# Performance work log

Hardware: AMD Instinct MI355X
Metric: run time of the kernel (lower is better)

## Reference

```python
import jax, jax.numpy as jnp
import numpy as np

B, D, K, A = 32768, 256, 1024, 32
MIN_LOG_STD, MAX_LOG_STD = -20.0, 2.0


def setup_inputs() -> dict:
    key = jax.random.key(0)
    ks = jax.random.split(key, 9)
    return {
        "obs": jax.random.normal(ks[0], (B, D), dtype=jnp.float32),
        "mean_C": jax.random.normal(ks[1], (K, D), dtype=jnp.float32),
        "mean_sigma": jnp.abs(jax.random.normal(ks[2], (K,), dtype=jnp.float32)) + 0.1,
        "mean_w": jax.random.normal(ks[3], (A, K), dtype=jnp.float32),
        "mean_b": jax.random.normal(ks[4], (A,), dtype=jnp.float32),
        "std_C": jax.random.normal(ks[5], (K, D), dtype=jnp.float32),
        "std_sigma": jnp.abs(jax.random.normal(ks[6], (K,), dtype=jnp.float32)) + 0.1,
        "std_w": jax.random.normal(ks[7], (A, K), dtype=jnp.float32),
        "std_b": jax.random.normal(ks[8], (A,), dtype=jnp.float32),
    }


def _rbf(x, C, sigma_sq, w, b):
    # r[b,k] = sum_d (x[b,d] - C[k,d])^2, expanded to avoid a [B,K,D] intermediate
    x2 = jnp.sum(x * x, axis=-1, keepdims=True)           # [B,1]
    c2 = jnp.sum(C * C, axis=-1)[None, :]                  # [1,K]
    r = x2 - 2.0 * (x @ C.T) + c2                          # [B,K]
    phi = jnp.exp(-r / (2.0 * jnp.abs(sigma_sq)[None, :]))  # [B,K]
    return phi @ w.T + b[None, :]                          # [B,A]


def reference(obs, mean_C, mean_sigma, mean_w, mean_b,
              std_C, std_sigma, std_w, std_b):
    action_mean = _rbf(obs, mean_C, mean_sigma, mean_w, mean_b)
    std_raw = _rbf(obs, std_C, std_sigma, std_w, std_b)
    action_std = jnp.exp(jnp.clip(std_raw, MIN_LOG_STD, MAX_LOG_STD))
    return jnp.concatenate((action_mean, action_std), axis=-1)  # [B, 2A]
```

## Files before the change

### kernel.cpp

```cpp
#include <hip/hip_runtime.h>


typedef float floatx4 __attribute__((ext_vector_type(4)));
typedef int   intx4  __attribute__((ext_vector_type(4)));
typedef unsigned int u32;
typedef unsigned char u8;

constexpr float LOG2E = 1.4426950408889634f;
constexpr float QS    = 25.4f;
constexpr float SINV2 = (5.0f / 127.0f) * (5.0f / 127.0f);

__device__ __forceinline__ u32 pk_fp8(float a, float b, float c, float d) {
  u32 v = __builtin_amdgcn_cvt_pk_fp8_f32(a, b, 0u, 0);
  v = __builtin_amdgcn_cvt_pk_fp8_f32(c, d, v, 1);
  return v;
}
__device__ __forceinline__ long mk64(u32 lo, u32 hi) {
  return (long)lo | ((long)hi << 32);
}
__device__ __forceinline__ int q8(float x) {
  return (int)rintf(fminf(fmaxf(x * QS, -127.f), 127.f));
}
__device__ __forceinline__ u32 pk_i8(int a, int b, int c, int d) {
  return (u32)(a & 255) | ((u32)(b & 255) << 8) | ((u32)(c & 255) << 16) | ((u32)(d & 255) << 24);
}

__global__ void prep(const float* __restrict__ mC, const float* __restrict__ mS,
                     const float* __restrict__ sC, const float* __restrict__ sS,
                     const float* __restrict__ mw, const float* __restrict__ sw,
                     u8* __restrict__ Cb2, float* __restrict__ a2g,
                     float* __restrict__ g2n, u8* __restrict__ wb)
{
  const int blk = blockIdx.x;
  if (blk < 512) {
    const int wq = threadIdx.x >> 6;
    const int t  = threadIdx.x & 63;
    const int b  = blk * 4 + wq;
    const int half = b >> 10;
    const int k = b & 1023;
    const float* src = (half ? sC : mC) + (size_t)k * 256;
    float4 f = *(const float4*)(src + t * 4);
    int i0 = q8(f.x), i1 = q8(f.y), i2 = q8(f.z), i3 = q8(f.w);
    const int ct = b >> 6, row = b & 63;
    const int wvv = row >> 4, cc = row & 15;
    const int ks = t >> 4, qq = (t >> 2) & 3, j0 = (t & 3) * 4;
    *(u32*)(Cb2 + (size_t)ct * 16384 + wvv * 4096 + (16 * qq + cc) * 64 + 16 * ks + j0) =
        pk_i8(i0, i1, i2, i3);
    int is = i0 * i0 + i1 * i1 + i2 * i2 + i3 * i3;
    for (int off = 32; off > 0; off >>= 1) is += __shfl_down(is, off, 64);
    if (t == 0) {
      float sig = fabsf((half ? sS : mS)[k]);
      float t2 = SINV2 * LOG2E * 0.5f / sig;
      a2g[b] = 2.f * t2;
      g2n[b] = -t2 * (float)is;
    }
  } else {
    int i0 = (blk - 512) * 1024 + threadIdx.x * 4;
    int half = i0 >> 15;
    int rem  = i0 & 32767;
    const float* src = half ? sw : mw;
    float4 f = *(const float4*)(src + rem);
    ((u32*)wb)[i0 >> 2] = pk_fp8(f.x, f.y, f.z, f.w);
  }
}

__global__ __launch_bounds__(256, 2)
void policy_main(const float* __restrict__ obs,
                 const u8* __restrict__ Cb2,
                 const float* __restrict__ a2g,
                 const float* __restrict__ g2n,
                 const u8* __restrict__ wb,
                 const float* __restrict__ mbias,
                 const float* __restrict__ sbias,
                 float* __restrict__ out)
{
  __shared__ __align__(16) char smem[69888];
  float* x2p = (float*)(smem + 16384);
  float* red = (float*)smem;

  const int tid  = threadIdx.x;
  const int lane = tid & 63;
  const int wv   = tid >> 6;
  const int c    = lane & 15;
  const int q    = lane >> 4;
  const int row0 = blockIdx.x * 64;
  const int kslc = 16 * wv + 4 * q;
  const int cfo  = tid * 64;

  intx4 cfPA[4], cfPB[4], cfQA[4], cfQB[4];
  #pragma unroll
  for (int i = 0; i < 4; ++i) {
    cfPA[i] = *(const intx4*)(Cb2 + cfo + i * 16);
    cfPB[i] = *(const intx4*)(Cb2 + 16384 + cfo + i * 16);
  }

  #pragma unroll
  for (int i = 0; i < 4; ++i) {
    int s = i * 256 + tid;
    int row = s >> 4;
    int s16 = s & 15;
    int l16 = s16 ^ (row & 15);
    const float* src = obs + (size_t)(row0 + row) * 256 + l16 * 16;
    float4 f0 = ((const float4*)src)[0];
    float4 f1 = ((const float4*)src)[1];
    float4 f2 = ((const float4*)src)[2];
    float4 f3 = ((const float4*)src)[3];
    int a0 = q8(f0.x), a1v = q8(f0.y), a2v = q8(f0.z), a3 = q8(f0.w);
    int b0 = q8(f1.x), b1 = q8(f1.y), b2 = q8(f1.z), b3 = q8(f1.w);
    int c0 = q8(f2.x), c1 = q8(f2.y), c2 = q8(f2.z), c3 = q8(f2.w);
    int d0 = q8(f3.x), d1 = q8(f3.y), d2 = q8(f3.z), d3 = q8(f3.w);
    uint4 pk;
    pk.x = pk_i8(a0, a1v, a2v, a3);
    pk.y = pk_i8(b0, b1, b2, b3);
    pk.z = pk_i8(c0, c1, c2, c3);
    pk.w = pk_i8(d0, d1, d2, d3);
    *(uint4*)(smem + s * 16) = pk;
    int is = a0*a0 + a1v*a1v + a2v*a2v + a3*a3
           + b0*b0 + b1*b1 + b2*b2 + b3*b3
           + c0*c0 + c1*c1 + c2*c2 + c3*c3
           + d0*d0 + d1*d1 + d2*d2 + d3*d3;
    x2p[row * 16 + s16] = (float)is;
  }
  __syncthreads();

  intx4 ob[4][4];
  #pragma unroll
  for (int nt = 0; nt < 4; ++nt) {
    const int row = nt * 16 + c;
    #pragma unroll
    for (int ks = 0; ks < 4; ++ks) {
      int slot = (4 * ks + q) ^ (row & 15);
      ob[nt][ks] = *(const intx4*)(smem + row * 256 + slot * 16);
    }
  }
  if (tid < 64) {
    float s = 0.f;
    #pragma unroll
    for (int j = 0; j < 16; j += 4) {
      float4 a = *(const float4*)(x2p + tid * 16 + j);
      s += a.x + a.y + a.z + a.w;
    }
    x2p[1024 + tid] = s;
  }
  __syncthreads();

  float hx2[4];
  #pragma unroll
  for (int nt = 0; nt < 4; ++nt) hx2[nt] = 0.5f * x2p[1024 + nt * 16 + c];

  const intx4 Z4i = {0, 0, 0, 0};
  const floatx4 Z4 = {0.f, 0.f, 0.f, 0.f};
  floatx4 acc2m[2][4], acc2s[2][4];
  #pragma unroll
  for (int a2i = 0; a2i < 2; ++a2i)
    #pragma unroll
    for (int nt = 0; nt < 4; ++nt) {
      acc2m[a2i][nt] = Z4;
      acc2s[a2i][nt] = Z4;
    }

  u32 pE[4], pc[4];

#define PAIR_BODY(pr, CA, CB, NA, NB, ACC, HB)                                          \
  {                                                                                     \
    const int cte = 2 * (pr);                                                           \
    if ((pr) < 15) {                                                                    \
      const u8* g0 = Cb2 + (size_t)(cte + 2) * 16384 + cfo;                             \
      _Pragma("unroll")                                                                 \
      for (int i = 0; i < 4; ++i) {                                                     \
        NA[i] = *(const intx4*)(g0 + i * 16);                                           \
        NB[i] = *(const intx4*)(g0 + 16384 + i * 16);                                   \
      }                                                                                 \
    }                                                                                   \
    float4 a2e = *(const float4*)(a2g + cte * 64 + kslc);                               \
    float4 g2e = *(const float4*)(g2n + cte * 64 + kslc);                               \
    float4 a2o = *(const float4*)(a2g + cte * 64 + 64 + kslc);                          \
    float4 g2o = *(const float4*)(g2n + cte * 64 + 64 + kslc);                          \
    const int kbE = (cte & 15) * 64 + kslc;                                             \
    const u8* wr0 = wb + (size_t)((HB) + c) * 1024 + kbE;                               \
    const u8* wr1 = wb + (size_t)((HB) + 16 + c) * 1024 + kbE;                          \
    u32 w0lo = *(const u32*)wr0, w0hi = *(const u32*)(wr0 + 64);                        \
    u32 w1lo = *(const u32*)wr1, w1hi = *(const u32*)(wr1 + 64);                        \
    intx4 a1[4];                                                                        \
    a1[0] = __builtin_amdgcn_mfma_i32_16x16x64_i8(CA[0], ob[0][0], Z4i, 0, 0, 0);       \
    a1[1] = __builtin_amdgcn_mfma_i32_16x16x64_i8(CA[0], ob[1][0], Z4i, 0, 0, 0);       \
    a1[2] = __builtin_amdgcn_mfma_i32_16x16x64_i8(CA[0], ob[2][0], Z4i, 0, 0, 0);       \
    a1[3] = __builtin_amdgcn_mfma_i32_16x16x64_i8(CA[0], ob[3][0], Z4i, 0, 0, 0);       \
    _Pragma("unroll")                                                                   \
    for (int ks = 1; ks < 4; ++ks) {                                                    \
      a1[0] = __builtin_amdgcn_mfma_i32_16x16x64_i8(CA[ks], ob[0][ks], a1[0], 0, 0, 0); \
      a1[1] = __builtin_amdgcn_mfma_i32_16x16x64_i8(CA[ks], ob[1][ks], a1[1], 0, 0, 0); \
      a1[2] = __builtin_amdgcn_mfma_i32_16x16x64_i8(CA[ks], ob[2][ks], a1[2], 0, 0, 0); \
      a1[3] = __builtin_amdgcn_mfma_i32_16x16x64_i8(CA[ks], ob[3][ks], a1[3], 0, 0, 0); \
    }                                                                                   \
    _Pragma("unroll")                                                                   \
    for (int nt = 0; nt < 4; ++nt) {                                                    \
      float t0 = (float)a1[nt][0] - hx2[nt], t1 = (float)a1[nt][1] - hx2[nt];           \
      float t2 = (float)a1[nt][2] - hx2[nt], t3 = (float)a1[nt][3] - hx2[nt];           \
      pE[nt] = pk_fp8(__builtin_amdgcn_exp2f(fmaf(a2e.x, t0, g2e.x)),                   \
                      __builtin_amdgcn_exp2f(fmaf(a2e.y, t1, g2e.y)),                   \
                      __builtin_amdgcn_exp2f(fmaf(a2e.z, t2, g2e.z)),                   \
                      __builtin_amdgcn_exp2f(fmaf(a2e.w, t3, g2e.w)));                  \
    }                                                                                   \
    a1[0] = __builtin_amdgcn_mfma_i32_16x16x64_i8(CB[0], ob[0][0], Z4i, 0, 0, 0);       \
    a1[1] = __builtin_amdgcn_mfma_i32_16x16x64_i8(CB[0], ob[1][0], Z4i, 0, 0, 0);       \
    a1[2] = __builtin_amdgcn_mfma_i32_16x16x64_i8(CB[0], ob[2][0], Z4i, 0, 0, 0);       \
    a1[3] = __builtin_amdgcn_mfma_i32_16x16x64_i8(CB[0], ob[3][0], Z4i, 0, 0, 0);       \
    _Pragma("unroll")                                                                   \
    for (int ks = 1; ks < 4; ++ks) {                                                    \
      a1[0] = __builtin_amdgcn_mfma_i32_16x16x64_i8(CB[ks], ob[0][ks], a1[0], 0, 0, 0); \
      a1[1] = __builtin_amdgcn_mfma_i32_16x16x64_i8(CB[ks], ob[1][ks], a1[1], 0, 0, 0); \
      a1[2] = __builtin_amdgcn_mfma_i32_16x16x64_i8(CB[ks], ob[2][ks], a1[2], 0, 0, 0); \
      a1[3] = __builtin_amdgcn_mfma_i32_16x16x64_i8(CB[ks], ob[3][ks], a1[3], 0, 0, 0); \
    }                                                                                   \
    _Pragma("unroll")                                                                   \
    for (int nt = 0; nt < 4; ++nt) {                                                    \
      float t0 = (float)a1[nt][0] - hx2[nt], t1 = (float)a1[nt][1] - hx2[nt];           \
      float t2 = (float)a1[nt][2] - hx2[nt], t3 = (float)a1[nt][3] - hx2[nt];           \
      pc[nt] = pk_fp8(__builtin_amdgcn_exp2f(fmaf(a2o.x, t0, g2o.x)),                   \
                      __builtin_amdgcn_exp2f(fmaf(a2o.y, t1, g2o.y)),                   \
                      __builtin_amdgcn_exp2f(fmaf(a2o.z, t2, g2o.z)),                   \
                      __builtin_amdgcn_exp2f(fmaf(a2o.w, t3, g2o.w)));                  \
    }                                                                                   \
    { long wA0 = mk64(w0lo, w0hi), wA1 = mk64(w1lo, w1hi);                              \
      _Pragma("unroll")                                                                 \
      for (int nt = 0; nt < 4; ++nt) {                                                  \
        long pb = mk64(pE[nt], pc[nt]);                                                 \
        ACC[0][nt] = __builtin_amdgcn_mfma_f32_16x16x32_fp8_fp8(wA0, pb, ACC[0][nt], 0, 0, 0); \
        ACC[1][nt] = __builtin_amdgcn_mfma_f32_16x16x32_fp8_fp8(wA1, pb, ACC[1][nt], 0, 0, 0); \
      } }                                                                               \
  }

  for (int pr = 0; pr < 8; pr += 2) {
    PAIR_BODY(pr,     cfPA, cfPB, cfQA, cfQB, acc2m, 0)
    PAIR_BODY(pr + 1, cfQA, cfQB, cfPA, cfPB, acc2m, 0)
  }
  for (int pr = 8; pr < 16; pr += 2) {
    PAIR_BODY(pr,     cfPA, cfPB, cfQA, cfQB, acc2s, 32)
    PAIR_BODY(pr + 1, cfQA, cfQB, cfPA, cfPB, acc2s, 32)
  }
#undef PAIR_BODY

  {
    float* myr = red + wv * 4352;
    #pragma unroll
    for (int a2i = 0; a2i < 2; ++a2i)
      #pragma unroll
      for (int nt = 0; nt < 4; ++nt) {
        *(floatx4*)(myr + (nt * 16 + c) * 68 + a2i * 16 + 4 * q)      = acc2m[a2i][nt];
        *(floatx4*)(myr + (nt * 16 + c) * 68 + 32 + a2i * 16 + 4 * q) = acc2s[a2i][nt];
      }
  }
  __syncthreads();

  #pragma unroll
  for (int i = 0; i < 16; ++i) {
    int idx = tid + 256 * i;
    int a = idx & 63;
    int b = idx >> 6;
    float v = red[b * 68 + a] + red[4352 + b * 68 + a] +
              red[8704 + b * 68 + a] + red[13056 + b * 68 + a];
    if (a < 32) {
      v += mbias[a];
    } else {
      v += sbias[a - 32];
      v = fminf(fmaxf(v, -20.f), 2.f);
      v = __builtin_amdgcn_exp2f(v * LOG2E);
    }
    out[(size_t)(row0 + b) * 64 + a] = v;
  }
}

extern "C" void kernel_launch(void* const* d_in, const int* in_sizes, int n_in,
                              void* d_out, int out_size, void* d_ws, size_t ws_size,
                              hipStream_t stream) {
  const float* obs = (const float*)d_in[0];
  const float* mC  = (const float*)d_in[1];
  const float* mS  = (const float*)d_in[2];
  const float* mW  = (const float*)d_in[3];
  const float* mB  = (const float*)d_in[4];
  const float* sC  = (const float*)d_in[5];
  const float* sS  = (const float*)d_in[6];
  const float* sW  = (const float*)d_in[7];
  const float* sB  = (const float*)d_in[8];
  float* out = (float*)d_out;

  u8*    Cb2 = (u8*)d_ws;
  float* a2g = (float*)((char*)d_ws + 2048 * 256);
  float* g2n = a2g + 2048;
  u8*    wb  = (u8*)(g2n + 2048);

  prep<<<576, 256, 0, stream>>>(mC, mS, sC, sS, mW, sW, Cb2, a2g, g2n, wb);
  policy_main<<<512, 256, 0, stream>>>(obs, Cb2, a2g, g2n, wb, mB, sB, out);
}
```

Measured before the change: 128.2 us.

## Software-pipeline GEMM1 tiles so exp of one tile overlaps next tile's MFMAs

Result: no change. 129.2 us (+0.8%).

```diff
diff --git a/kernel.cpp b/kernel.cpp
--- a/kernel.cpp
+++ b/kernel.cpp
@@ -87,12 +87,16 @@
   const int kslc = 16 * wv + 4 * q;
   const int cfo  = tid * 64;
 
-  intx4 cfPA[4], cfPB[4], cfQA[4], cfQB[4];
-  #pragma unroll
-  for (int i = 0; i < 4; ++i) {
-    cfPA[i] = *(const intx4*)(Cb2 + cfo + i * 16);
-    cfPB[i] = *(const intx4*)(Cb2 + 16384 + cfo + i * 16);
-  }
+#define LOADCF(CF, t)                                                     \
+  { const u8* g0_ = Cb2 + (size_t)(t) * 16384 + cfo;                      \
+    CF[0] = *(const intx4*)(g0_);                                         \
+    CF[1] = *(const intx4*)(g0_ + 16);                                    \
+    CF[2] = *(const intx4*)(g0_ + 32);                                    \
+    CF[3] = *(const intx4*)(g0_ + 48); }
+
+  intx4 cfU[4], cfV[4];
+  LOADCF(cfU, 0)
+  LOADCF(cfV, 1)
 
   #pragma unroll
   for (int i = 0; i < 4; ++i) {
@@ -159,87 +163,91 @@
       acc2s[a2i][nt] = Z4;
     }
 
+  intx4 a1A[4], a1B[4];
+  float4 acA, gcA, acB, gcB;
   u32 pE[4], pc[4];
 
-#define PAIR_BODY(pr, CA, CB, NA, NB, ACC, HB)                                          \
-  {                                                                                     \
-    const int cte = 2 * (pr);                                                           \
-    if ((pr) < 15) {                                                                    \
-      const u8* g0 = Cb2 + (size_t)(cte + 2) * 16384 + cfo;                             \
-      _Pragma("unroll")                                                                 \
-      for (int i = 0; i < 4; ++i) {                                                     \
-        NA[i] = *(const intx4*)(g0 + i * 16);                                           \
-        NB[i] = *(const intx4*)(g0 + 16384 + i * 16);                                   \
-      }                                                                                 \
-    }                                                                                   \
-    float4 a2e = *(const float4*)(a2g + cte * 64 + kslc);                               \
-    float4 g2e = *(const float4*)(g2n + cte * 64 + kslc);                               \
-    float4 a2o = *(const float4*)(a2g + cte * 64 + 64 + kslc);                          \
-    float4 g2o = *(const float4*)(g2n + cte * 64 + 64 + kslc);                          \
-    const int kbE = (cte & 15) * 64 + kslc;                                             \
-    const u8* wr0 = wb + (size_t)((HB) + c) * 1024 + kbE;                               \
-    const u8* wr1 = wb + (size_t)((HB) + 16 + c) * 1024 + kbE;                          \
-    u32 w0lo = *(const u32*)wr0, w0hi = *(const u32*)(wr0 + 64);                        \
-    u32 w1lo = *(const u32*)wr1, w1hi = *(const u32*)(wr1 + 64);                        \
-    intx4 a1[4];                                                                        \
-    a1[0] = __builtin_amdgcn_mfma_i32_16x16x64_i8(CA[0], ob[0][0], Z4i, 0, 0, 0);       \
-    a1[1] = __builtin_amdgcn_mfma_i32_16x16x64_i8(CA[0], ob[1][0], Z4i, 0, 0, 0);       \
-    a1[2] = __builtin_amdgcn_mfma_i32_16x16x64_i8(CA[0], ob[2][0], Z4i, 0, 0, 0);       \
-    a1[3] = __builtin_amdgcn_mfma_i32_16x16x64_i8(CA[0], ob[3][0], Z4i, 0, 0, 0);       \
-    _Pragma("unroll")                                                                   \
-    for (int ks = 1; ks < 4; ++ks) {                                                    \
-      a1[0] = __builtin_amdgcn_mfma_i32_16x16x64_i8(CA[ks], ob[0][ks], a1[0], 0, 0, 0); \
-      a1[1] = __builtin_amdgcn_mfma_i32_16x16x64_i8(CA[ks], ob[1][ks], a1[1], 0, 0, 0); \
-      a1[2] = __builtin_amdgcn_mfma_i32_16x16x64_i8(CA[ks], ob[2][ks], a1[2], 0, 0, 0); \
-      a1[3] = __builtin_amdgcn_mfma_i32_16x16x64_i8(CA[ks], ob[3][ks], a1[3], 0, 0, 0); \
-    }                                                                                   \
-    _Pragma("unroll")                                                                   \
-    for (int nt = 0; nt < 4; ++nt) {                                                    \
-      float t0 = (float)a1[nt][0] - hx2[nt], t1 = (float)a1[nt][1] - hx2[nt];           \
-      float t2 = (float)a1[nt][2] - hx2[nt], t3 = (float)a1[nt][3] - hx2[nt];           \
-      pE[nt] = pk_fp8(__builtin_amdgcn_exp2f(fmaf(a2e.x, t0, g2e.x)),                   \
-                      __builtin_amdgcn_exp2f(fmaf(a2e.y, t1, g2e.y)),                   \
-                      __builtin_amdgcn_exp2f(fmaf(a2e.z, t2, g2e.z)),                   \
-                      __builtin_amdgcn_exp2f(fmaf(a2e.w, t3, g2e.w)));                  \
-    }                                                                                   \
-    a1[0] = __builtin_amdgcn_mfma_i32_16x16x64_i8(CB[0], ob[0][0], Z4i, 0, 0, 0);       \
-    a1[1] = __builtin_amdgcn_mfma_i32_16x16x64_i8(CB[0], ob[1][0], Z4i, 0, 0, 0);       \
-    a1[2] = __builtin_amdgcn_mfma_i32_16x16x64_i8(CB[0], ob[2][0], Z4i, 0, 0, 0);       \
-    a1[3] = __builtin_amdgcn_mfma_i32_16x16x64_i8(CB[0], ob[3][0], Z4i, 0, 0, 0);       \
-    _Pragma("unroll")                                                                   \
-    for (int ks = 1; ks < 4; ++ks) {                                                    \
-      a1[0] = __builtin_amdgcn_mfma_i32_16x16x64_i8(CB[ks], ob[0][ks], a1[0], 0, 0, 0); \
-      a1[1] = __builtin_amdgcn_mfma_i32_16x16x64_i8(CB[ks], ob[1][ks], a1[1], 0, 0, 0); \
-      a1[2] = __builtin_amdgcn_mfma_i32_16x16x64_i8(CB[ks], ob[2][ks], a1[2], 0, 0, 0); \
-      a1[3] = __builtin_amdgcn_mfma_i32_16x16x64_i8(CB[ks], ob[3][ks], a1[3], 0, 0, 0); \
-    }                                                                                   \
-    _Pragma("unroll")                                                                   \
-    for (int nt = 0; nt < 4; ++nt) {                                                    \
-      float t0 = (float)a1[nt][0] - hx2[nt], t1 = (float)a1[nt][1] - hx2[nt];           \
-      float t2 = (float)a1[nt][2] - hx2[nt], t3 = (float)a1[nt][3] - hx2[nt];           \
-      pc[nt] = pk_fp8(__builtin_amdgcn_exp2f(fmaf(a2o.x, t0, g2o.x)),                   \
-                      __builtin_amdgcn_exp2f(fmaf(a2o.y, t1, g2o.y)),                   \
-                      __builtin_amdgcn_exp2f(fmaf(a2o.z, t2, g2o.z)),                   \
-                      __builtin_amdgcn_exp2f(fmaf(a2o.w, t3, g2o.w)));                  \
-    }                                                                                   \
-    { long wA0 = mk64(w0lo, w0hi), wA1 = mk64(w1lo, w1hi);                              \
-      _Pragma("unroll")                                                                 \
-      for (int nt = 0; nt < 4; ++nt) {                                                  \
-        long pb = mk64(pE[nt], pc[nt]);                                                 \
-        ACC[0][nt] = __builtin_amdgcn_mfma_f32_16x16x32_fp8_fp8(wA0, pb, ACC[0][nt], 0, 0, 0); \
-        ACC[1][nt] = __builtin_amdgcn_mfma_f32_16x16x32_fp8_fp8(wA1, pb, ACC[1][nt], 0, 0, 0); \
-      } }                                                                               \
-  }
-
-  for (int pr = 0; pr < 8; pr += 2) {
-    PAIR_BODY(pr,     cfPA, cfPB, cfQA, cfQB, acc2m, 0)
-    PAIR_BODY(pr + 1, cfQA, cfQB, cfPA, cfPB, acc2m, 0)
-  }
-  for (int pr = 8; pr < 16; pr += 2) {
-    PAIR_BODY(pr,     cfPA, cfPB, cfQA, cfQB, acc2s, 32)
-    PAIR_BODY(pr + 1, cfQA, cfQB, cfPA, cfPB, acc2s, 32)
-  }
-#undef PAIR_BODY
+#define GEMM1T(CF, A1)                                                          \
+  { A1[0] = __builtin_amdgcn_mfma_i32_16x16x64_i8(CF[0], ob[0][0], Z4i, 0, 0, 0); \
+    A1[1] = __builtin_amdgcn_mfma_i32_16x16x64_i8(CF[0], ob[1][0], Z4i, 0, 0, 0); \
+    A1[2] = __builtin_amdgcn_mfma_i32_16x16x64_i8(CF[0], ob[2][0], Z4i, 0, 0, 0); \
+    A1[3] = __builtin_amdgcn_mfma_i32_16x16x64_i8(CF[0], ob[3][0], Z4i, 0, 0, 0); \
+    _Pragma("unroll")                                                           \
+    for (int ks = 1; ks < 4; ++ks) {                                            \
+      A1[0] = __builtin_amdgcn_mfma_i32_16x16x64_i8(CF[ks], ob[0][ks], A1[0], 0, 0, 0); \
+      A1[1] = __builtin_amdgcn_mfma_i32_16x16x64_i8(CF[ks], ob[1][ks], A1[1], 0, 0, 0); \
+      A1[2] = __builtin_amdgcn_mfma_i32_16x16x64_i8(CF[ks], ob[2][ks], A1[2], 0, 0, 0); \
+      A1[3] = __builtin_amdgcn_mfma_i32_16x16x64_i8(CF[ks], ob[3][ks], A1[3], 0, 0, 0); \
+    } }
+
+#define EXPP(A1, AC, GC, DST)                                                   \
+  { _Pragma("unroll")                                                           \
+    for (int nt = 0; nt < 4; ++nt) {                                            \
+      float t0 = (float)A1[nt][0] - hx2[nt], t1 = (float)A1[nt][1] - hx2[nt];   \
+      float t2 = (float)A1[nt][2] - hx2[nt], t3 = (float)A1[nt][3] - hx2[nt];   \
+      DST[nt] = pk_fp8(__builtin_amdgcn_exp2f(fmaf(AC.x, t0, GC.x)),            \
+                       __builtin_amdgcn_exp2f(fmaf(AC.y, t1, GC.y)),            \
+                       __builtin_amdgcn_exp2f(fmaf(AC.z, t2, GC.z)),            \
+                       __builtin_amdgcn_exp2f(fmaf(AC.w, t3, GC.w))); } }
+
+#define GEMM2P(ACC, W0L, W0H, W1L, W1H)                                         \
+  { long wA0 = mk64(W0L, W0H), wA1 = mk64(W1L, W1H);                            \
+    _Pragma("unroll")                                                           \
+    for (int nt = 0; nt < 4; ++nt) {                                            \
+      long pb = mk64(pE[nt], pc[nt]);                                           \
+      ACC[0][nt] = __builtin_amdgcn_mfma_f32_16x16x32_fp8_fp8(wA0, pb, ACC[0][nt], 0, 0, 0); \
+      ACC[1][nt] = __builtin_amdgcn_mfma_f32_16x16x32_fp8_fp8(wA1, pb, ACC[1][nt], 0, 0, 0); \
+    } }
+
+  acA = *(const float4*)(a2g + kslc);
+  gcA = *(const float4*)(g2n + kslc);
+  GEMM1T(cfU, a1A)
+  LOADCF(cfU, 2)
+
+#define STEP(m, ACC, HB, DO_U)                                                  \
+  {                                                                             \
+    const int e = 2 * (m);                                                      \
+    const int kbE = (e & 15) * 64 + kslc;                                       \
+    const u8* wr0 = wb + (size_t)((HB) + c) * 1024 + kbE;                       \
+    const u8* wr1 = wb + (size_t)((HB) + 16 + c) * 1024 + kbE;                  \
+    u32 w0lo = *(const u32*)wr0, w0hi = *(const u32*)(wr0 + 64);                \
+    u32 w1lo = *(const u32*)wr1, w1hi = *(const u32*)(wr1 + 64);                \
+    acB = *(const float4*)(a2g + (e + 1) * 64 + kslc);                          \
+    gcB = *(const float4*)(g2n + (e + 1) * 64 + kslc);                          \
+    GEMM1T(cfV, a1B)                                                            \
+    LOADCF(cfV, e + 3)                                                          \
+    EXPP(a1A, acA, gcA, pE)                                                     \
+    acA = *(const float4*)(a2g + (e + 2) * 64 + kslc);                          \
+    gcA = *(const float4*)(g2n + (e + 2) * 64 + kslc);                          \
+    GEMM1T(cfU, a1A)                                                            \
+    if (DO_U) LOADCF(cfU, e + 4)                                                \
+    EXPP(a1B, acB, gcB, pc)                                                     \
+    GEMM2P(ACC, w0lo, w0hi, w1lo, w1hi)                                         \
+  }
+
+  #pragma unroll
+  for (int m = 0; m < 8; ++m) STEP(m, acc2m, 0, 1)
+  #pragma unroll
+  for (int m = 8; m < 14; ++m) STEP(m, acc2s, 32, 1)
+  STEP(14, acc2s, 32, 0)
+  {
+    const int kbE = (30 & 15) * 64 + kslc;
+    const u8* wr0 = wb + (size_t)(32 + c) * 1024 + kbE;
+    const u8* wr1 = wb + (size_t)(48 + c) * 1024 + kbE;
+    u32 w0lo = *(const u32*)wr0, w0hi = *(const u32*)(wr0 + 64);
+    u32 w1lo = *(const u32*)wr1, w1hi = *(const u32*)(wr1 + 64);
+    acB = *(const float4*)(a2g + 31 * 64 + kslc);
+    gcB = *(const float4*)(g2n + 31 * 64 + kslc);
+    GEMM1T(cfV, a1B)
+    EXPP(a1A, acA, gcA, pE)
+    EXPP(a1B, acB, gcB, pc)
+    GEMM2P(acc2s, w0lo, w0hi, w1lo, w1hi)
+  }
+#undef STEP
+#undef GEMM1T
+#undef EXPP
+#undef GEMM2P
+#undef LOADCF
 
   {
     float* myr = red + wv * 4352;
```
